# Kernel tuning notes

Hardware: AMD Instinct MI355X
Metric: run time of the kernel (lower is better)

Reference implementation:

```python
import jax, jax.numpy as jnp
import numpy as np

EPS = 1e-6  # epsilon used to snap near-zero plane distances (Moller-style robustness)


def _interval(p, d):
    """Interval of the intersection line covered by a triangle.
    p: [..., 3] projections of the 3 vertices onto the intersection-line axis.
    d: [..., 3] signed distances of the 3 vertices to the other triangle's plane.
    Returns (tmin, tmax); invalid (non-straddling) -> (+inf, -inf).
    """
    nxt = jnp.array([1, 2, 0])
    di, dj = d, d[..., nxt]
    pi, pj = p, p[..., nxt]
    # edge crosses the plane iff endpoint distances have opposite signs
    # (or exactly one endpoint lies on the plane)
    valid = (di * dj <= 0) & ~((di == 0) & (dj == 0))
    denom = di - dj
    t = pi + (pj - pi) * di / jnp.where(denom == 0, 1.0, denom)
    tmin = jnp.min(jnp.where(valid, t, jnp.inf), axis=-1)
    tmax = jnp.max(jnp.where(valid, t, -jnp.inf), axis=-1)
    return tmin, tmax


def _pairwise_intersect(T):
    """Moller-style triangle-triangle intersection test for all N^2 pairs.
    T: [N, 3, 3] triangle soup. Returns bool [N, N].
    """
    N = T.shape[0]
    n = jnp.cross(T[:, 1] - T[:, 0], T[:, 2] - T[:, 0])   # [N,3] plane normals
    d = -jnp.sum(n * T[:, 0], axis=-1)                      # [N] plane offsets
    # signed distances: verts of triangle b to plane of triangle u (dv), and vice versa (du)
    dv = jnp.einsum('bvc,nc->bnv', T, n) + d[None, :, None]  # [N,N,3]
    du = jnp.einsum('nvc,bc->bnv', T, n) + d[:, None, None]  # [N,N,3]
    dv = jnp.where(jnp.abs(dv) < EPS, 0.0, dv)
    du = jnp.where(jnp.abs(du) < EPS, 0.0, du)
    # all vertices strictly on one side -> no intersection
    ssv = jnp.all(dv > 0, -1) | jnp.all(dv < 0, -1)
    ssu = jnp.all(du > 0, -1) | jnp.all(du < 0, -1)
    # direction of plane-plane intersection line; project onto its dominant axis
    D = jnp.cross(n[:, None, :], n[None, :, :])              # [N,N,3]
    ax = jnp.argmax(jnp.abs(D), axis=-1)                     # [N,N]
    idx = jnp.broadcast_to(ax[..., None, None], (N, N, 3, 1))
    pv = jnp.take_along_axis(jnp.broadcast_to(T[:, None], (N, N, 3, 3)), idx, -1)[..., 0]
    pu = jnp.take_along_axis(jnp.broadcast_to(T[None, :], (N, N, 3, 3)), idx, -1)[..., 0]
    t0v, t1v = _interval(pv, dv)
    t0u, t1u = _interval(pu, du)
    overlap = jnp.maximum(t0v, t0u) <= jnp.minimum(t1v, t1u)
    return ~ssv & ~ssu & overlap


def setup_inputs() -> dict:
    key = jax.random.key(0)
    triangles = jax.random.normal(key, (2048, 3, 3), dtype=jnp.float32)
    return {"triangles": triangles}


def reference(triangles):
    # CPU extension produces the strictly-upper-triangular pairwise matrix;
    # the torch wrapper symmetrizes it and adds the identity.
    N = triangles.shape[0]
    M = _pairwise_intersect(triangles).astype(jnp.float32)
    S = jnp.triu(M, 1)
    return S + S.T + jnp.eye(N, dtype=jnp.float32)
```

## Files before the change

### kernel.cpp

```cpp
#include <hip/hip_runtime.h>
#include <math.h>


static constexpr float EPS_SNAP = 1e-6f;
static constexpr int TS = 32;

__device__ __forceinline__ float snapz(float x) {
    return (fabsf(x) < EPS_SNAP) ? 0.0f : x;
}

__device__ __forceinline__ void tri_interval(const float p[3], const float d[3],
                                             float& tmin, float& tmax) {
#pragma clang fp contract(off)
    tmin = INFINITY;
    tmax = -INFINITY;
#pragma unroll
    for (int e = 0; e < 3; ++e) {
        const int i0 = e;
        const int i1 = (e + 1) % 3;
        const float di = d[i0], dj = d[i1];
        const float pi = p[i0], pj = p[i1];
        const bool valid = (di * dj <= 0.0f) && !((di == 0.0f) && (dj == 0.0f));
        const float denom = di - dj;
        const float dsafe = (denom == 0.0f) ? 1.0f : denom;
        const float t = pi + ((pj - pi) * di) / dsafe;
        if (valid) {
            tmin = fminf(tmin, t);
            tmax = fmaxf(tmax, t);
        }
    }
}

__global__ __launch_bounds__(256, 8) void tile_kernel(
    const float* __restrict__ tri, float* __restrict__ out, int n)
{
#pragma clang fp contract(off)
    const int nt = n / TS;
    int k = blockIdx.x, tr = 0;
    while (k >= nt - tr) { k -= nt - tr; ++tr; }
    const int tc = tr + k;
    const int R = tr * TS, C = tc * TS;

    __shared__ float Asf[TS * 12];
    __shared__ float Bsf[TS * 12];
    __shared__ float4 Apl[TS], Bpl[TS];
    __shared__ float Sres[TS][TS + 1];
    __shared__ unsigned short qbuf[TS * TS];
    __shared__ int s_cnt;

    const int tx = threadIdx.x;
    const int ty = threadIdx.y;
    const int t = ty * TS + tx;
    const int lane = t & 63;

    if (t == 0) s_cnt = 0;
    for (int g = t; g < TS * 9; g += 256) {
        const int a = g / 9, c9 = g - a * 9;
        Asf[a * 12 + c9] = tri[(size_t)R * 9 + g];
        Bsf[a * 12 + c9] = tri[(size_t)C * 9 + g];
    }
    if (t < 2 * TS) {
        const int idx = (t < TS) ? (R + t) : (C + (t - TS));
        const float* V = tri + (size_t)idx * 9;
        float Vv[9];
#pragma unroll
        for (int q = 0; q < 9; ++q) Vv[q] = V[q];
        const float e1x = Vv[3] - Vv[0], e1y = Vv[4] - Vv[1], e1z = Vv[5] - Vv[2];
        const float e2x = Vv[6] - Vv[0], e2y = Vv[7] - Vv[1], e2z = Vv[8] - Vv[2];
        const float nx = e1y * e2z - e1z * e2y;
        const float ny = e1z * e2x - e1x * e2z;
        const float nz = e1x * e2y - e1y * e2x;
        const float d = -(((nx * Vv[0]) + (ny * Vv[1])) + (nz * Vv[2]));
        if (t < TS) Apl[t] = make_float4(nx, ny, nz, d);
        else        Bpl[t - TS] = make_float4(nx, ny, nz, d);
    }
    __syncthreads();

    float Bv[9];
    {
        const float4 b0 = *(const float4*)&Bsf[tx * 12];
        const float4 b1 = *(const float4*)&Bsf[tx * 12 + 4];
        Bv[0] = b0.x; Bv[1] = b0.y; Bv[2] = b0.z; Bv[3] = b0.w;
        Bv[4] = b1.x; Bv[5] = b1.y; Bv[6] = b1.z; Bv[7] = b1.w;
        Bv[8] = Bsf[tx * 12 + 8];
    }
    const float4 pb = Bpl[tx];

    for (int kk = 0; kk < 4; ++kk) {
        const int r = ty + 8 * kk;
        const float4 a0 = *(const float4*)&Asf[r * 12];
        const float4 a1 = *(const float4*)&Asf[r * 12 + 4];
        const float a8 = Asf[r * 12 + 8];
        const float4 pa = Apl[r];
        const float dv0 = (((a0.x * pb.x) + (a0.y * pb.y)) + (a0.z * pb.z)) + pb.w;
        const float dv1 = (((a0.w * pb.x) + (a1.x * pb.y)) + (a1.y * pb.z)) + pb.w;
        const float dv2 = (((a1.z * pb.x) + (a1.w * pb.y)) + (a8 * pb.z)) + pb.w;
        const float du0 = (((Bv[0] * pa.x) + (Bv[1] * pa.y)) + (Bv[2] * pa.z)) + pa.w;
        const float du1 = (((Bv[3] * pa.x) + (Bv[4] * pa.y)) + (Bv[5] * pa.z)) + pa.w;
        const float du2 = (((Bv[6] * pa.x) + (Bv[7] * pa.y)) + (Bv[8] * pa.z)) + pa.w;
        const float mnv = fminf(fminf(dv0, dv1), dv2), mxv = fmaxf(fmaxf(dv0, dv1), dv2);
        const float mnu = fminf(fminf(du0, du1), du2), mxu = fmaxf(fmaxf(du0, du1), du2);
        const bool ssv = (mnv >= EPS_SNAP) || (mxv <= -EPS_SNAP);
        const bool ssu = (mnu >= EPS_SNAP) || (mxu <= -EPS_SNAP);
        const int i = R + r, j = C + tx;
        const bool surv = !ssv && !ssu && (i != j);
        Sres[r][tx] = (i == j) ? 1.0f : 0.0f;
        const unsigned long long m = __ballot(surv);
        int wb = 0;
        if (lane == 0) {
            const int wcnt = __popcll(m);
            if (wcnt) wb = atomicAdd(&s_cnt, wcnt);
        }
        wb = __shfl(wb, 0);
        if (surv) {
            const int pos = wb + __popcll(m & ((1ull << lane) - 1ull));
            qbuf[pos] = (unsigned short)((r << 5) | tx);
        }
    }
    __syncthreads();

    const int total = s_cnt;
    for (int q = t; q < total; q += 256) {
        const int e = qbuf[q];
        const int r = e >> 5, c = e & 31;

        const float4 pa = Apl[r];
        const float4 pq = Bpl[c];
        const float nax = pa.x, nay = pa.y, naz = pa.z, da = pa.w;
        const float nbx = pq.x, nby = pq.y, nbz = pq.z, db = pq.w;

        float dv[3], du[3];
        {
            const float4 a0 = *(const float4*)&Asf[r * 12];
            const float4 a1 = *(const float4*)&Asf[r * 12 + 4];
            const float a8 = Asf[r * 12 + 8];
            dv[0] = snapz((((a0.x * nbx) + (a0.y * nby)) + (a0.z * nbz)) + db);
            dv[1] = snapz((((a0.w * nbx) + (a1.x * nby)) + (a1.y * nbz)) + db);
            dv[2] = snapz((((a1.z * nbx) + (a1.w * nby)) + (a8 * nbz)) + db);
            const float4 b0 = *(const float4*)&Bsf[c * 12];
            const float4 b1 = *(const float4*)&Bsf[c * 12 + 4];
            const float b8 = Bsf[c * 12 + 8];
            du[0] = snapz((((b0.x * nax) + (b0.y * nay)) + (b0.z * naz)) + da);
            du[1] = snapz((((b0.w * nax) + (b1.x * nay)) + (b1.y * naz)) + da);
            du[2] = snapz((((b1.z * nax) + (b1.w * nay)) + (b8 * naz)) + da);
        }

        const float Dx = nay * nbz - naz * nby;
        const float Dy = naz * nbx - nax * nbz;
        const float Dz = nax * nby - nay * nbx;
        const float m0 = fabsf(Dx), m1 = fabsf(Dy), m2 = fabsf(Dz);
        int axm = 0;
        float mm = m0;
        if (m1 > mm) { axm = 1; mm = m1; }
        if (m2 > mm) { axm = 2; }

        float pv[3], pu[3];
#pragma unroll
        for (int v = 0; v < 3; ++v) {
            pv[v] = Asf[r * 12 + 3 * v + axm];
            pu[v] = Bsf[c * 12 + 3 * v + axm];
        }

        float t0v, t1v, t0u, t1u;
        tri_interval(pv, dv, t0v, t1v);
        tri_interval(pu, du, t0u, t1u);

        const bool overlap = fmaxf(t0v, t0u) <= fminf(t1v, t1u);
        Sres[r][c] = overlap ? 1.0f : 0.0f;
    }
    __syncthreads();

    {
        const int row = t >> 3;
        const int c4 = (t & 7) * 4;
        float4 v;
        v.x = Sres[row][c4 + 0]; v.y = Sres[row][c4 + 1];
        v.z = Sres[row][c4 + 2]; v.w = Sres[row][c4 + 3];
        *(float4*)&out[(size_t)(R + row) * n + C + c4] = v;
        if (tr != tc) {
            float4 w;
            w.x = Sres[c4 + 0][row]; w.y = Sres[c4 + 1][row];
            w.z = Sres[c4 + 2][row]; w.w = Sres[c4 + 3][row];
            *(float4*)&out[(size_t)(C + row) * n + R + c4] = w;
        }
    }
}

extern "C" void kernel_launch(void* const* d_in, const int* in_sizes, int n_in,
                              void* d_out, int out_size, void* d_ws, size_t ws_size,
                              hipStream_t stream) {
    const float* tri = (const float*)d_in[0];
    float* out = (float*)d_out;
    const int n = in_sizes[0] / 9;

    const int nt = n / TS;
    const int nblocks = nt * (nt + 1) / 2;
    dim3 block(TS, 8);
    tile_kernel<<<nblocks, block, 0, stream>>>(tri, out, n);
}
```

Baseline: 71.20 us.

## Use FMA prefilter with error-bounded threshold and specialized straddle interval

The prefilter now computes plane distances with fused multiply-adds and rejects pairs using a per-tile threshold scaled by the maximum vertex and normal magnitudes. Because that conservative bound can let extra pairs through, an exact same-side test is added on the survivor path. The three-edge interval loop is replaced by a closed-form version that picks the lone vertex, with the original loop kept as a fallback when any distance is zero. The per-tile statistics reduction adds a barrier, and a looser threshold may send more pairs to the survivor path. The launch-bounds occupancy hint is lowered from 8 to 6.

```diff
diff --git a/kernel.cpp b/kernel.cpp
--- a/kernel.cpp
+++ b/kernel.cpp
@@ -31,7 +31,24 @@
     }
 }
 
-__global__ __launch_bounds__(256, 8) void tile_kernel(
+__device__ __forceinline__ void tri_interval2(const float p[3], const float d[3],
+                                              float& tmin, float& tmax) {
+#pragma clang fp contract(off)
+    const bool s0 = d[0] > 0.0f, s1 = d[1] > 0.0f, s2 = d[2] > 0.0f;
+    const int o = (s0 == s1) ? 2 : ((s1 == s2) ? 0 : 1);
+    const float po = (o == 0) ? p[0] : ((o == 1) ? p[1] : p[2]);
+    const float dO = (o == 0) ? d[0] : ((o == 1) ? d[1] : d[2]);
+    const float pj = (o == 0) ? p[1] : ((o == 1) ? p[2] : p[0]);
+    const float dj = (o == 0) ? d[1] : ((o == 1) ? d[2] : d[0]);
+    const float pi = (o == 0) ? p[2] : ((o == 1) ? p[0] : p[1]);
+    const float di = (o == 0) ? d[2] : ((o == 1) ? d[0] : d[1]);
+    const float tA = po + ((pj - po) * dO) / (dO - dj);
+    const float tB = pi + ((po - pi) * di) / (di - dO);
+    tmin = fminf(tA, tB);
+    tmax = fmaxf(tA, tB);
+}
+
+__global__ __launch_bounds__(256, 6) void tile_kernel(
     const float* __restrict__ tri, float* __restrict__ out, int n)
 {
 #pragma clang fp contract(off)
@@ -46,6 +63,7 @@
     __shared__ float4 Apl[TS], Bpl[TS];
     __shared__ float Sres[TS][TS + 1];
     __shared__ unsigned short qbuf[TS * TS];
+    __shared__ float tstat[4];
     __shared__ int s_cnt;
 
     const int tx = threadIdx.x;
@@ -76,6 +94,29 @@
     }
     __syncthreads();
 
+    {
+        const int w = t >> 6;
+        float lm = 0.0f;
+        if (w < 2) {
+            const float* S = (w == 0) ? Asf : Bsf;
+            const int row = lane & 31, half = lane >> 5;
+            const int base = row * 12 + half * 5;
+            const int cnt = half ? 4 : 5;
+            for (int q = 0; q < cnt; ++q) lm = fmaxf(lm, fabsf(S[base + q]));
+        } else if (lane < TS) {
+            const float4 p = (w == 2) ? Apl[lane] : Bpl[lane];
+            lm = fmaxf(fmaxf(fabsf(p.x), fabsf(p.y)), fabsf(p.z));
+        }
+#pragma unroll
+        for (int off = 32; off > 0; off >>= 1) lm = fmaxf(lm, __shfl_xor(lm, off));
+        if (lane == 0) tstat[w] = lm;
+    }
+    __syncthreads();
+
+    const float sumM = tstat[0] + tstat[1];
+    const float thrV = EPS_SNAP + 6e-6f * (tstat[3] * sumM);
+    const float thrU = EPS_SNAP + 6e-6f * (tstat[2] * sumM);
+
     float Bv[9];
     {
         const float4 b0 = *(const float4*)&Bsf[tx * 12];
@@ -92,18 +133,18 @@
         const float4 a1 = *(const float4*)&Asf[r * 12 + 4];
         const float a8 = Asf[r * 12 + 8];
         const float4 pa = Apl[r];
-        const float dv0 = (((a0.x * pb.x) + (a0.y * pb.y)) + (a0.z * pb.z)) + pb.w;
-        const float dv1 = (((a0.w * pb.x) + (a1.x * pb.y)) + (a1.y * pb.z)) + pb.w;
-        const float dv2 = (((a1.z * pb.x) + (a1.w * pb.y)) + (a8 * pb.z)) + pb.w;
-        const float du0 = (((Bv[0] * pa.x) + (Bv[1] * pa.y)) + (Bv[2] * pa.z)) + pa.w;
-        const float du1 = (((Bv[3] * pa.x) + (Bv[4] * pa.y)) + (Bv[5] * pa.z)) + pa.w;
-        const float du2 = (((Bv[6] * pa.x) + (Bv[7] * pa.y)) + (Bv[8] * pa.z)) + pa.w;
+        const float dv0 = fmaf(a0.x, pb.x, fmaf(a0.y, pb.y, fmaf(a0.z, pb.z, pb.w)));
+        const float dv1 = fmaf(a0.w, pb.x, fmaf(a1.x, pb.y, fmaf(a1.y, pb.z, pb.w)));
+        const float dv2 = fmaf(a1.z, pb.x, fmaf(a1.w, pb.y, fmaf(a8, pb.z, pb.w)));
+        const float du0 = fmaf(Bv[0], pa.x, fmaf(Bv[1], pa.y, fmaf(Bv[2], pa.z, pa.w)));
+        const float du1 = fmaf(Bv[3], pa.x, fmaf(Bv[4], pa.y, fmaf(Bv[5], pa.z, pa.w)));
+        const float du2 = fmaf(Bv[6], pa.x, fmaf(Bv[7], pa.y, fmaf(Bv[8], pa.z, pa.w)));
         const float mnv = fminf(fminf(dv0, dv1), dv2), mxv = fmaxf(fmaxf(dv0, dv1), dv2);
         const float mnu = fminf(fminf(du0, du1), du2), mxu = fmaxf(fmaxf(du0, du1), du2);
-        const bool ssv = (mnv >= EPS_SNAP) || (mxv <= -EPS_SNAP);
-        const bool ssu = (mnu >= EPS_SNAP) || (mxu <= -EPS_SNAP);
+        const bool rejv = (mnv >= thrV) || (mxv <= -thrV);
+        const bool reju = (mnu >= thrU) || (mxu <= -thrU);
         const int i = R + r, j = C + tx;
-        const bool surv = !ssv && !ssu && (i != j);
+        const bool surv = !rejv && !reju && (i != j);
         Sres[r][tx] = (i == j) ? 1.0f : 0.0f;
         const unsigned long long m = __ballot(surv);
         int wb = 0;
@@ -145,6 +186,11 @@
             du[2] = snapz((((b1.z * nax) + (b1.w * nay)) + (b8 * naz)) + da);
         }
 
+        const bool ssv = (dv[0] > 0.0f && dv[1] > 0.0f && dv[2] > 0.0f) ||
+                         (dv[0] < 0.0f && dv[1] < 0.0f && dv[2] < 0.0f);
+        const bool ssu = (du[0] > 0.0f && du[1] > 0.0f && du[2] > 0.0f) ||
+                         (du[0] < 0.0f && du[1] < 0.0f && du[2] < 0.0f);
+
         const float Dx = nay * nbz - naz * nby;
         const float Dy = naz * nbx - nax * nbz;
         const float Dz = nax * nby - nay * nbx;
@@ -162,11 +208,15 @@
         }
 
         float t0v, t1v, t0u, t1u;
-        tri_interval(pv, dv, t0v, t1v);
-        tri_interval(pu, du, t0u, t1u);
+        tri_interval2(pv, dv, t0v, t1v);
+        tri_interval2(pu, du, t0u, t1u);
+        const bool hzA = (dv[0] == 0.0f) || (dv[1] == 0.0f) || (dv[2] == 0.0f);
+        const bool hzB = (du[0] == 0.0f) || (du[1] == 0.0f) || (du[2] == 0.0f);
+        if (hzA) tri_interval(pv, dv, t0v, t1v);
+        if (hzB) tri_interval(pu, du, t0u, t1u);
 
         const bool overlap = fmaxf(t0v, t0u) <= fminf(t1v, t1u);
-        Sres[r][c] = overlap ? 1.0f : 0.0f;
+        Sres[r][c] = (!ssv && !ssu && overlap) ? 1.0f : 0.0f;
     }
     __syncthreads();
 
```

Result: no change. 71.40 us (+0.3%).
